# Performance work log

Measured on AMD Instinct MI355X. Metric: run time of the kernel, lower is better.

Reference implementation:

```python
import jax, jax.numpy as jnp
import numpy as np


def setup_inputs() -> dict:
    key = jax.random.key(0)
    k1, k2 = jax.random.split(key)
    num_tokens, top_k, num_experts = 1048576, 8, 64
    top_scores = jax.random.uniform(k1, (num_tokens, top_k), dtype=jnp.float32)
    selected_experts_indices = jax.random.randint(
        k2, (num_tokens, top_k), 0, num_experts, dtype=jnp.int64
    ) if jax.config.jax_enable_x64 else jax.random.randint(
        k2, (num_tokens, top_k), 0, num_experts, dtype=jnp.int32
    )
    return {
        "top_scores": top_scores,
        "selected_experts_indices": selected_experts_indices,
        "num_experts": num_experts,
    }


def reference(top_scores, selected_experts_indices, num_experts):
    flat_idx = selected_experts_indices.reshape(-1)  # [num_tokens*top_k]
    # histogram of tokens per expert (torch.histc returns float)
    num_tokens_per_expert = jnp.bincount(flat_idx, length=num_experts).astype(jnp.float32)
    # stable argsort by expert id -> permutation grouping tokens by expert
    token_indices_experts_sorted = jnp.argsort(flat_idx, stable=True)
    # gather routing scores into expert-sorted order
    top_scores_experts_sorted = top_scores.reshape(-1)[token_indices_experts_sorted]
    return (
        top_scores_experts_sorted,
        token_indices_experts_sorted,
        num_tokens_per_expert,
    )
```

## Files before the change

kernel.cpp:

```cpp
#include <hip/hip_runtime.h>


#define TILE 4096
#define WCH  1024
#define RND  16

__device__ __forceinline__ unsigned long long match_mask(
    unsigned key,
    unsigned long long b0, unsigned long long b1, unsigned long long b2,
    unsigned long long b3, unsigned long long b4, unsigned long long b5,
    unsigned long long am) {
  unsigned long long m = am;
  m &= (key & 1u)  ? b0 : ~b0;
  m &= (key & 2u)  ? b1 : ~b1;
  m &= (key & 4u)  ? b2 : ~b2;
  m &= (key & 8u)  ? b3 : ~b3;
  m &= (key & 16u) ? b4 : ~b4;
  m &= (key & 32u) ? b5 : ~b5;
  return m;
}

__global__ __launch_bounds__(256) void hist_kernel(
    const int* __restrict__ idx, unsigned* __restrict__ countsT,
    int N, int nb) {
  __shared__ unsigned h[4][64];
  const int wave = threadIdx.x >> 6;
  const int lane = threadIdx.x & 63;

  long long base = (long long)blockIdx.x * TILE;
  long long rem = (long long)N - base;
  unsigned cnt = 0;

  if (rem >= TILE) {
    const int4* v = (const int4*)(idx + base);
    unsigned es[16];
    #pragma unroll
    for (int k = 0; k < 4; ++k) {
      int4 x = v[threadIdx.x + k * 256];
      es[k * 4 + 0] = ((unsigned)x.x) & 63u;
      es[k * 4 + 1] = ((unsigned)x.y) & 63u;
      es[k * 4 + 2] = ((unsigned)x.z) & 63u;
      es[k * 4 + 3] = ((unsigned)x.w) & 63u;
    }
    #pragma unroll
    for (int r = 0; r < 16; ++r) {
      unsigned e = es[r];
      unsigned long long b0 = __ballot(e & 1u);
      unsigned long long b1 = __ballot(e & 2u);
      unsigned long long b2 = __ballot(e & 4u);
      unsigned long long b3 = __ballot(e & 8u);
      unsigned long long b4 = __ballot(e & 16u);
      unsigned long long b5 = __ballot(e & 32u);
      cnt += (unsigned)__popcll(
          match_mask((unsigned)lane, b0, b1, b2, b3, b4, b5, ~0ull));
    }
  } else {
    long long wstart = base + (long long)wave * WCH;
    for (int r = 0; r < RND; ++r) {
      long long i = wstart + (long long)r * 64 + lane;
      bool valid = i < (long long)N;
      unsigned long long am = __ballot(valid ? 1 : 0);
      unsigned e = valid ? (((unsigned)idx[i]) & 63u) : 0u;
      unsigned long long b0 = __ballot(e & 1u);
      unsigned long long b1 = __ballot(e & 2u);
      unsigned long long b2 = __ballot(e & 4u);
      unsigned long long b3 = __ballot(e & 8u);
      unsigned long long b4 = __ballot(e & 16u);
      unsigned long long b5 = __ballot(e & 32u);
      cnt += (unsigned)__popcll(
          match_mask((unsigned)lane, b0, b1, b2, b3, b4, b5, am));
    }
  }

  h[wave][lane] = cnt;
  __syncthreads();
  if (threadIdx.x < 64) {
    countsT[(size_t)threadIdx.x * nb + blockIdx.x] =
        h[0][threadIdx.x] + h[1][threadIdx.x] + h[2][threadIdx.x] + h[3][threadIdx.x];
  }
}

__global__ __launch_bounds__(256) void scan_kernel(
    unsigned* __restrict__ countsT, unsigned* __restrict__ totals,
    float* __restrict__ out_counts, int nb) {
  const int e = blockIdx.x;
  const int t = threadIdx.x;
  const int wave = t >> 6;
  const int lane = t & 63;
  unsigned* row = countsT + (size_t)e * nb;

  __shared__ unsigned buf[2048];
  __shared__ unsigned wsum[4];

  unsigned carry = 0;
  for (int c = 0; c < nb; c += 2048) {
    int m = nb - c; if (m > 2048) m = 2048;
    for (int j = t; j < 2048; j += 256) buf[j] = (j < m) ? row[c + j] : 0u;
    __syncthreads();
    unsigned v[8]; unsigned s = 0;
    #pragma unroll
    for (int k = 0; k < 8; ++k) { v[k] = buf[t * 8 + k]; s += v[k]; }
    unsigned inc = s;
    #pragma unroll
    for (int d = 1; d < 64; d <<= 1) {
      unsigned nv = __shfl_up(inc, d, 64);
      if (lane >= d) inc += nv;
    }
    if (lane == 63) wsum[wave] = inc;
    __syncthreads();
    unsigned woff = 0;
    for (int w = 0; w < wave; ++w) woff += wsum[w];
    unsigned btot = wsum[0] + wsum[1] + wsum[2] + wsum[3];
    unsigned run = carry + woff + (inc - s);
    #pragma unroll
    for (int k = 0; k < 8; ++k) { buf[t * 8 + k] = run; run += v[k]; }
    __syncthreads();
    for (int j = t; j < 2048; j += 256) if (j < m) row[c + j] = buf[j];
    carry += btot;
    __syncthreads();
  }
  if (t == 0) {
    totals[e] = carry;
    out_counts[e] = (float)carry;
  }
}

__global__ __launch_bounds__(256, 4) void scatter_kernel(
    const int* __restrict__ idx, const float* __restrict__ scores,
    const unsigned* __restrict__ baseT, const unsigned* __restrict__ totals,
    float* __restrict__ out_scores, float* __restrict__ out_idx,
    int N, int nb) {
  __shared__ uint2    sdat[TILE];
  __shared__ unsigned shc[4][64];
  __shared__ unsigned gdest[64];

  const int wave = threadIdx.x >> 6;
  const int lane = threadIdx.x & 63;
  const unsigned long long lt = (1ull << lane) - 1ull;

  const long long start = (long long)blockIdx.x * TILE + (long long)wave * WCH;
  const bool fullt = ((long long)(blockIdx.x + 1) * TILE) <= (long long)N;

  const unsigned tot = totals[lane];
  const unsigned gb0 = baseT[(size_t)lane * nb + blockIdx.x];

  unsigned e_pk[4] = {0, 0, 0, 0};
  unsigned r_pk[4] = {0, 0, 0, 0};
  unsigned c_pk[4] = {0, 0, 0, 0};
  float    sreg[RND];
  unsigned wtotal = 0;

  if (fullt) {
    #pragma unroll
    for (int r = 0; r < RND; ++r) {
      long long i = start + r * 64 + lane;
      unsigned e = ((unsigned)idx[i]) & 63u;
      sreg[r] = scores[i];
      unsigned long long b0 = __ballot(e & 1u);
      unsigned long long b1 = __ballot(e & 2u);
      unsigned long long b2 = __ballot(e & 4u);
      unsigned long long b3 = __ballot(e & 8u);
      unsigned long long b4 = __ballot(e & 16u);
      unsigned long long b5 = __ballot(e & 32u);
      unsigned long long ms = match_mask(e, b0, b1, b2, b3, b4, b5, ~0ull);
      unsigned rank = (unsigned)__popcll(ms & lt);
      unsigned cnt  = (unsigned)__popcll(
          match_mask((unsigned)lane, b0, b1, b2, b3, b4, b5, ~0ull));
      const int q = r >> 2, sh = (r & 3) * 8;
      e_pk[q] |= e << sh;
      r_pk[q] |= rank << sh;
      c_pk[q] |= cnt << sh;
      wtotal += cnt;
    }
  } else {
    for (int j = threadIdx.x; j < TILE; j += 256) sdat[j].y = 0xFFFFFFFFu;
    __syncthreads();
    for (int r = 0; r < RND; ++r) {
      long long i = start + (long long)r * 64 + lane;
      bool valid = i < (long long)N;
      unsigned long long am = __ballot(valid ? 1 : 0);
      unsigned e = valid ? (((unsigned)idx[i]) & 63u) : 0u;
      sreg[r] = valid ? scores[i] : 0.0f;
      unsigned long long b0 = __ballot(e & 1u);
      unsigned long long b1 = __ballot(e & 2u);
      unsigned long long b2 = __ballot(e & 4u);
      unsigned long long b3 = __ballot(e & 8u);
      unsigned long long b4 = __ballot(e & 16u);
      unsigned long long b5 = __ballot(e & 32u);
      unsigned long long ms = match_mask(e, b0, b1, b2, b3, b4, b5, am);
      unsigned rank = (unsigned)__popcll(ms & lt);
      unsigned cnt  = (unsigned)__popcll(
          match_mask((unsigned)lane, b0, b1, b2, b3, b4, b5, am));
      const int q = r >> 2, sh = (r & 3) * 8;
      e_pk[q] |= e << sh;
      r_pk[q] |= rank << sh;
      c_pk[q] |= cnt << sh;
      wtotal += cnt;
    }
  }

  shc[wave][lane] = wtotal;
  __syncthreads();

  unsigned c0 = shc[0][lane], c1 = shc[1][lane];
  unsigned c2 = shc[2][lane], c3 = shc[3][lane];
  unsigned bt = c0 + c1 + c2 + c3;
  unsigned wpre = 0;
  if (wave > 0) wpre += c0;
  if (wave > 1) wpre += c1;
  if (wave > 2) wpre += c2;

  unsigned s = bt;
  #pragma unroll
  for (int d = 1; d < 64; d <<= 1) {
    unsigned nv = __shfl_up(s, d, 64);
    if (lane >= d) s += nv;
  }
  unsigned bstart = s - bt;
  unsigned wbase = bstart + wpre;

  unsigned cur[RND];
  {
    unsigned acc = wbase;
    #pragma unroll
    for (int r = 0; r < RND; ++r) {
      cur[r] = acc;
      acc += (c_pk[r >> 2] >> ((r & 3) * 8)) & 0xffu;
    }
  }

  if (wave == 0) {
    unsigned s2 = tot;
    #pragma unroll
    for (int d = 1; d < 64; d <<= 1) {
      unsigned nv = __shfl_up(s2, d, 64);
      if (lane >= d) s2 += nv;
    }
    unsigned estart = s2 - tot;
    gdest[lane] = estart + gb0 - bstart;
  }

  if (fullt) {
    #pragma unroll
    for (int r = 0; r < RND; ++r) {
      unsigned i32 = (unsigned)(start + r * 64 + lane);
      const int q = r >> 2, sh = (r & 3) * 8;
      unsigned e    = (e_pk[q] >> sh) & 0xffu;
      unsigned rank = (r_pk[q] >> sh) & 0xffu;
      unsigned pos = (unsigned)__shfl((int)cur[r], (int)e, 64) + rank;
      sdat[pos] = make_uint2(__float_as_uint(sreg[r]), (i32 << 6) | e);
    }
  } else {
    for (int r = 0; r < RND; ++r) {
      long long i = start + (long long)r * 64 + lane;
      bool valid = i < (long long)N;
      const int q = r >> 2, sh = (r & 3) * 8;
      unsigned e    = (e_pk[q] >> sh) & 0xffu;
      unsigned rank = (r_pk[q] >> sh) & 0xffu;
      unsigned pos = (unsigned)__shfl((int)cur[r], (int)e, 64) + rank;
      if (valid) {
        sdat[pos] = make_uint2(__float_as_uint(sreg[r]), (((unsigned)i) << 6) | e);
      }
    }
  }
  __syncthreads();

  if (fullt) {
    #pragma unroll
    for (int k = 0; k < TILE / 256; ++k) {
      int j = threadIdx.x + k * 256;
      uint2 v = sdat[j];
      unsigned e = v.y & 63u;
      unsigned d = gdest[e] + (unsigned)j;
      out_scores[d] = __uint_as_float(v.x);
      out_idx[d] = (float)(v.y >> 6);
    }
  } else {
    for (int j = threadIdx.x; j < TILE; j += 256) {
      uint2 v = sdat[j];
      if (v.y == 0xFFFFFFFFu) continue;
      unsigned e = v.y & 63u;
      unsigned d = gdest[e] + (unsigned)j;
      out_scores[d] = __uint_as_float(v.x);
      out_idx[d] = (float)(v.y >> 6);
    }
  }
}

extern "C" void kernel_launch(void* const* d_in, const int* in_sizes, int n_in,
                              void* d_out, int out_size, void* d_ws, size_t ws_size,
                              hipStream_t stream) {
  const float* scores = (const float*)d_in[0];
  const int* idx = (const int*)d_in[1];
  int N = in_sizes[0];

  float* out_scores = (float*)d_out;
  float* out_idx = out_scores + N;
  float* out_counts = out_idx + N;

  int nb = (N + TILE - 1) / TILE;
  unsigned* countsT = (unsigned*)d_ws;
  unsigned* totals = countsT + (size_t)64 * nb;

  hist_kernel<<<nb, 256, 0, stream>>>(idx, countsT, N, nb);
  scan_kernel<<<64, 256, 0, stream>>>(countsT, totals, out_counts, nb);
  scatter_kernel<<<nb, 256, 0, stream>>>(idx, scores, countsT, totals,
                                         out_scores, out_idx, N, nb);
}
```

Baseline: 142.5 us.

## Halve tile size, transpose count layout, and compute per-expert counts via shared bytes

Tiles shrink from 4096 to 2048 elements, with 8 rounds per wave, and the scatter kernel's occupancy hint rises to 8 blocks. The per-block count matrix becomes block-major, so the histogram and scatter kernels write and read it contiguously, while the scan kernel now reads it with a 64-element stride. In the scatter kernel, indices are staged through shared memory using vectorized int4 loads. Per-expert counts are now written as bytes by each group leader into a shared table, replacing the second match_mask/popcount per round. The trade-offs are twice as many blocks and a longer scan, strided global access in the scan, and extra barriers and shared-memory traffic.

```diff
diff --git a/kernel.cpp b/kernel.cpp
--- a/kernel.cpp
+++ b/kernel.cpp
@@ -1,9 +1,9 @@
 #include <hip/hip_runtime.h>
 
 
-#define TILE 4096
-#define WCH  1024
-#define RND  16
+#define TILE 2048
+#define WCH  512
+#define RND  8
 
 __device__ __forceinline__ unsigned long long match_mask(
     unsigned key,
@@ -33,17 +33,15 @@
 
   if (rem >= TILE) {
     const int4* v = (const int4*)(idx + base);
-    unsigned es[16];
-    #pragma unroll
-    for (int k = 0; k < 4; ++k) {
-      int4 x = v[threadIdx.x + k * 256];
-      es[k * 4 + 0] = ((unsigned)x.x) & 63u;
-      es[k * 4 + 1] = ((unsigned)x.y) & 63u;
-      es[k * 4 + 2] = ((unsigned)x.z) & 63u;
-      es[k * 4 + 3] = ((unsigned)x.w) & 63u;
-    }
-    #pragma unroll
-    for (int r = 0; r < 16; ++r) {
+    int4 x0 = v[threadIdx.x];
+    int4 x1 = v[threadIdx.x + 256];
+    unsigned es[8] = {
+        ((unsigned)x0.x) & 63u, ((unsigned)x0.y) & 63u,
+        ((unsigned)x0.z) & 63u, ((unsigned)x0.w) & 63u,
+        ((unsigned)x1.x) & 63u, ((unsigned)x1.y) & 63u,
+        ((unsigned)x1.z) & 63u, ((unsigned)x1.w) & 63u};
+    #pragma unroll
+    for (int r = 0; r < 8; ++r) {
       unsigned e = es[r];
       unsigned long long b0 = __ballot(e & 1u);
       unsigned long long b1 = __ballot(e & 2u);
@@ -75,7 +73,7 @@
   h[wave][lane] = cnt;
   __syncthreads();
   if (threadIdx.x < 64) {
-    countsT[(size_t)threadIdx.x * nb + blockIdx.x] =
+    countsT[(size_t)blockIdx.x * 64 + threadIdx.x] =
         h[0][threadIdx.x] + h[1][threadIdx.x] + h[2][threadIdx.x] + h[3][threadIdx.x];
   }
 }
@@ -87,7 +85,6 @@
   const int t = threadIdx.x;
   const int wave = t >> 6;
   const int lane = t & 63;
-  unsigned* row = countsT + (size_t)e * nb;
 
   __shared__ unsigned buf[2048];
   __shared__ unsigned wsum[4];
@@ -95,7 +92,8 @@
   unsigned carry = 0;
   for (int c = 0; c < nb; c += 2048) {
     int m = nb - c; if (m > 2048) m = 2048;
-    for (int j = t; j < 2048; j += 256) buf[j] = (j < m) ? row[c + j] : 0u;
+    for (int j = t; j < 2048; j += 256)
+      buf[j] = (j < m) ? countsT[(size_t)(c + j) * 64 + e] : 0u;
     __syncthreads();
     unsigned v[8]; unsigned s = 0;
     #pragma unroll
@@ -115,7 +113,8 @@
     #pragma unroll
     for (int k = 0; k < 8; ++k) { buf[t * 8 + k] = run; run += v[k]; }
     __syncthreads();
-    for (int j = t; j < 2048; j += 256) if (j < m) row[c + j] = buf[j];
+    for (int j = t; j < 2048; j += 256)
+      if (j < m) countsT[(size_t)(c + j) * 64 + e] = buf[j];
     carry += btot;
     __syncthreads();
   }
@@ -125,37 +124,52 @@
   }
 }
 
-__global__ __launch_bounds__(256, 4) void scatter_kernel(
+__global__ __launch_bounds__(256, 8) void scatter_kernel(
     const int* __restrict__ idx, const float* __restrict__ scores,
     const unsigned* __restrict__ baseT, const unsigned* __restrict__ totals,
     float* __restrict__ out_scores, float* __restrict__ out_idx,
     int N, int nb) {
-  __shared__ uint2    sdat[TILE];
+  __shared__ __align__(16) uint2 sdat[TILE];
+  __shared__ __align__(16) unsigned char tmpb[4][64][RND];
   __shared__ unsigned shc[4][64];
   __shared__ unsigned gdest[64];
 
-  const int wave = threadIdx.x >> 6;
-  const int lane = threadIdx.x & 63;
+  const int t = threadIdx.x;
+  const int wave = t >> 6;
+  const int lane = t & 63;
   const unsigned long long lt = (1ull << lane) - 1ull;
 
-  const long long start = (long long)blockIdx.x * TILE + (long long)wave * WCH;
-  const bool fullt = ((long long)(blockIdx.x + 1) * TILE) <= (long long)N;
+  const long long base = (long long)blockIdx.x * TILE;
+  const long long start = base + (long long)wave * WCH;
+  const bool fullt = (base + TILE) <= (long long)N;
 
   const unsigned tot = totals[lane];
-  const unsigned gb0 = baseT[(size_t)lane * nb + blockIdx.x];
-
-  unsigned e_pk[4] = {0, 0, 0, 0};
-  unsigned r_pk[4] = {0, 0, 0, 0};
-  unsigned c_pk[4] = {0, 0, 0, 0};
+  const unsigned gb0 = baseT[(size_t)blockIdx.x * 64 + lane];
+
+  unsigned e_pk[2] = {0, 0};
+  unsigned r_pk[2] = {0, 0};
   float    sreg[RND];
+  unsigned c_pk[2];
   unsigned wtotal = 0;
 
+  unsigned* idxs = (unsigned*)sdat;
+
   if (fullt) {
-    #pragma unroll
-    for (int r = 0; r < RND; ++r) {
-      long long i = start + r * 64 + lane;
-      unsigned e = ((unsigned)idx[i]) & 63u;
-      sreg[r] = scores[i];
+    {
+      const int4* gi = (const int4*)(idx + base);
+      int4 a = gi[t];
+      int4 b = gi[t + 256];
+      #pragma unroll
+      for (int r = 0; r < RND; ++r) sreg[r] = scores[start + r * 64 + lane];
+      ((int4*)idxs)[t] = a;
+      ((int4*)idxs)[t + 256] = b;
+    }
+    *(uint2*)(&tmpb[wave][lane][0]) = make_uint2(0u, 0u);
+    __syncthreads();
+
+    #pragma unroll
+    for (int r = 0; r < RND; ++r) {
+      unsigned e = idxs[wave * WCH + r * 64 + lane] & 63u;
       unsigned long long b0 = __ballot(e & 1u);
       unsigned long long b1 = __ballot(e & 2u);
       unsigned long long b2 = __ballot(e & 4u);
@@ -164,16 +178,17 @@
       unsigned long long b5 = __ballot(e & 32u);
       unsigned long long ms = match_mask(e, b0, b1, b2, b3, b4, b5, ~0ull);
       unsigned rank = (unsigned)__popcll(ms & lt);
-      unsigned cnt  = (unsigned)__popcll(
-          match_mask((unsigned)lane, b0, b1, b2, b3, b4, b5, ~0ull));
+      unsigned rcnt = (unsigned)__popcll(ms);
+      if (rank == 0) tmpb[wave][e][r] = (unsigned char)rcnt;
       const int q = r >> 2, sh = (r & 3) * 8;
       e_pk[q] |= e << sh;
       r_pk[q] |= rank << sh;
-      c_pk[q] |= cnt << sh;
-      wtotal += cnt;
-    }
+    }
+    uint2 cw = *(const uint2*)(&tmpb[wave][lane][0]);
+    c_pk[0] = cw.x; c_pk[1] = cw.y;
   } else {
-    for (int j = threadIdx.x; j < TILE; j += 256) sdat[j].y = 0xFFFFFFFFu;
+    for (int j = t; j < TILE; j += 256) sdat[j].y = 0xFFFFFFFFu;
+    *(uint2*)(&tmpb[wave][lane][0]) = make_uint2(0u, 0u);
     __syncthreads();
     for (int r = 0; r < RND; ++r) {
       long long i = start + (long long)r * 64 + lane;
@@ -189,14 +204,20 @@
       unsigned long long b5 = __ballot(e & 32u);
       unsigned long long ms = match_mask(e, b0, b1, b2, b3, b4, b5, am);
       unsigned rank = (unsigned)__popcll(ms & lt);
-      unsigned cnt  = (unsigned)__popcll(
-          match_mask((unsigned)lane, b0, b1, b2, b3, b4, b5, am));
+      unsigned rcnt = (unsigned)__popcll(ms);
+      if (valid && rank == 0) tmpb[wave][e][r] = (unsigned char)rcnt;
       const int q = r >> 2, sh = (r & 3) * 8;
       e_pk[q] |= e << sh;
       r_pk[q] |= rank << sh;
-      c_pk[q] |= cnt << sh;
-      wtotal += cnt;
-    }
+    }
+    uint2 cw = *(const uint2*)(&tmpb[wave][lane][0]);
+    c_pk[0] = cw.x; c_pk[1] = cw.y;
+  }
+
+  {
+    unsigned a = c_pk[0], b = c_pk[1];
+    wtotal = (a & 0xffu) + ((a >> 8) & 0xffu) + ((a >> 16) & 0xffu) + (a >> 24)
+           + (b & 0xffu) + ((b >> 8) & 0xffu) + ((b >> 16) & 0xffu) + (b >> 24);
   }
 
   shc[wave][lane] = wtotal;
@@ -243,7 +264,7 @@
   if (fullt) {
     #pragma unroll
     for (int r = 0; r < RND; ++r) {
-      unsigned i32 = (unsigned)(start + r * 64 + lane);
+      unsigned i32 = (unsigned)start + r * 64 + lane;
       const int q = r >> 2, sh = (r & 3) * 8;
       unsigned e    = (e_pk[q] >> sh) & 0xffu;
       unsigned rank = (r_pk[q] >> sh) & 0xffu;
@@ -268,7 +289,7 @@
   if (fullt) {
     #pragma unroll
     for (int k = 0; k < TILE / 256; ++k) {
-      int j = threadIdx.x + k * 256;
+      int j = t + k * 256;
       uint2 v = sdat[j];
       unsigned e = v.y & 63u;
       unsigned d = gdest[e] + (unsigned)j;
@@ -276,7 +297,7 @@
       out_idx[d] = (float)(v.y >> 6);
     }
   } else {
-    for (int j = threadIdx.x; j < TILE; j += 256) {
+    for (int j = t; j < TILE; j += 256) {
       uint2 v = sdat[j];
       if (v.y == 0xFFFFFFFFu) continue;
       unsigned e = v.y & 63u;
@@ -300,7 +321,7 @@
 
   int nb = (N + TILE - 1) / TILE;
   unsigned* countsT = (unsigned*)d_ws;
-  unsigned* totals = countsT + (size_t)64 * nb;
+  unsigned* totals = countsT + (size_t)nb * 64;
 
   hist_kernel<<<nb, 256, 0, stream>>>(idx, countsT, N, nb);
   scan_kernel<<<64, 256, 0, stream>>>(countsT, totals, out_counts, nb);
```

Measured after the change: 149.6 us. 1.05x slower.
